# Kernel optimization log

Measured on AMD Instinct MI355X. Metric: run time of the kernel, lower is better.

## Reference

```python
import jax, jax.numpy as jnp
import numpy as np

EPS = 1e-12


def _koleo_single(x):
    # x: [B, D]
    # F.normalize(p=2, dim=-1): x / max(||x||, eps)
    norm = jnp.linalg.norm(x, axis=-1, keepdims=True)
    xn = x / jnp.maximum(norm, EPS)
    # pairwise inner products [B, B], mask diagonal with -1
    dots = xn @ xn.T
    n = xn.shape[0]
    dots = jnp.where(jnp.eye(n, dtype=bool), -1.0, dots)
    I = jnp.argmax(dots, axis=1)  # nearest neighbor index per row
    # torch PairwiseDistance(2, eps): (sum (x - y + eps)^2)^(1/2)
    diff = xn - xn[I] + EPS
    distances = jnp.sqrt(jnp.sum(diff * diff, axis=-1))
    return -jnp.mean(jnp.log(distances + EPS))


def setup_inputs() -> dict:
    key = jax.random.key(0)
    episodes_vectors = jax.random.normal(key, (8192, 4, 1024), dtype=jnp.float32)
    return {"episodes_vectors": episodes_vectors}


def reference(episodes_vectors) -> jnp.ndarray:
    # [B, T, D] -> [T, B, D], one KoLeo loss per view, averaged
    x_tbd = jnp.transpose(episodes_vectors, (1, 0, 2))
    losses = jax.vmap(_koleo_single)(x_tbd)  # [T]
    return jnp.mean(losses)
```

## Files before the change

kernel.cpp:

```cpp
#include <hip/hip_runtime.h>
#include <hip/hip_bf16.h>
#include <math.h>

#define B_N 8192
#define T_N 4
#define D_N 1024
#define BM  128
#define BN  256
#define NT  16
#define NBLK 1056

typedef float f32x4 __attribute__((ext_vector_type(4)));
typedef long longx2 __attribute__((ext_vector_type(2)));

__device__ inline unsigned int f2u_ord(float f) {
    unsigned int b = __float_as_uint(f);
    return (b & 0x80000000u) ? ~b : (b | 0x80000000u);
}
__device__ inline float u2f_ord(unsigned int u) {
    unsigned int b = (u & 0x80000000u) ? (u & 0x7FFFFFFFu) : ~u;
    return __uint_as_float(b);
}

__device__ inline unsigned int f2e4m3(float f) {
    unsigned int u = __float_as_uint(f);
    unsigned int sgn = (u >> 24) & 0x80u;
    int e = (int)((u >> 23) & 0xFFu) - 127;
    unsigned int m = u & 0x7FFFFFu;
    if (e >= -6) {
        unsigned int mant = m >> 20;
        unsigned int rest = m & 0xFFFFFu;
        mant += (rest > 0x80000u) || (rest == 0x80000u && (mant & 1u));
        unsigned int exp8 = (unsigned)(e + 7);
        if (mant == 8u) { mant = 0u; exp8 += 1u; }
        return sgn | (exp8 << 3) | mant;
    } else {
        float a = fabsf(f) * 512.0f;
        int q = (int)rintf(a);
        if (q >= 8) return sgn | 0x08u;
        return sgn | (unsigned)q;
    }
}

__global__ __launch_bounds__(256) void init_rowmax_kernel(unsigned int* __restrict__ rowmax) {
    int i = blockIdx.x * 256 + threadIdx.x;
    if (i < T_N * B_N) rowmax[i] = 0u;
}

__global__ __launch_bounds__(256) void norm_kernel(const float* __restrict__ in,
                                                   unsigned char* __restrict__ xn) {
    const int row  = blockIdx.x * 4 + (threadIdx.x >> 6);
    const int lane = threadIdx.x & 63;
    const int b = row >> 2;
    const int t = row & 3;
    const float* src = in + (size_t)row * D_N;

    float4 v[4];
    float ss = 0.f;
#pragma unroll
    for (int i = 0; i < 4; ++i) {
        v[i] = reinterpret_cast<const float4*>(src)[lane + 64 * i];
        ss += v[i].x * v[i].x + v[i].y * v[i].y + v[i].z * v[i].z + v[i].w * v[i].w;
    }
#pragma unroll
    for (int off = 32; off; off >>= 1) ss += __shfl_xor(ss, off, 64);
    const float rn = 1.0f / fmaxf(sqrtf(ss), 1e-12f);

    unsigned int* dst = reinterpret_cast<unsigned int*>(xn + ((size_t)t * B_N + b) * D_N);
#pragma unroll
    for (int i = 0; i < 4; ++i) {
        unsigned int p = f2e4m3(v[i].x * rn) | (f2e4m3(v[i].y * rn) << 8) |
                         (f2e4m3(v[i].z * rn) << 16) | (f2e4m3(v[i].w * rn) << 24);
        const int w  = lane + 64 * i;
        const int pp = (((w >> 1) & 3) << 1) | ((w >> 3) & 1);
        const int dw = (w & ~15) | (pp << 1) | (w & 1);
        dst[dw] = p;
    }
}

#define GLOAD_LDS16(g, l)                                                              \
    __builtin_amdgcn_global_load_lds(                                                  \
        (const __attribute__((address_space(1))) unsigned int*)(g),                    \
        (__attribute__((address_space(3))) unsigned int*)(l), 16, 0, 0)

__global__ __launch_bounds__(512, 4) void gemm_rowmax_kernel(const unsigned char* __restrict__ xn,
                                                             unsigned int* __restrict__ rowmax) {
    const int t = blockIdx.z;
    const int bid = blockIdx.x;
    int l = (bid & 7) * (NBLK / 8) + (bid >> 3);
    int bx = 0;
    while (l >= 2 * bx + 2) { l -= 2 * bx + 2; ++bx; }
    const int by = l;

    const unsigned char* X = xn + (size_t)t * B_N * D_N;

    __shared__ __align__(16) unsigned char lds[73728];

    const int tid  = threadIdx.x;
    const int lane = tid & 63;
    const int wv   = tid >> 6;
    const int wm   = wv >> 2;
    const int wn   = wv & 3;

    const int srow = lane >> 2;
    const int spos = (lane & 3) ^ ((lane >> 4) & 3);
    const unsigned char* gA  = X + (size_t)(by * BM + wv * 16 + srow) * D_N + spos * 16;
    const unsigned char* gB0 = X + (size_t)(bx * BN + wv * 16 + srow) * D_N + spos * 16;
    const unsigned char* gB1 = gB0 + (size_t)128 * D_N;

    const unsigned rdoff = (unsigned)(lane & 15) * 64u +
                           (unsigned)(((lane >> 4) ^ (lane >> 2)) & 3) * 16u;

    f32x4 acc[4][4];
#pragma unroll
    for (int m = 0; m < 4; ++m)
#pragma unroll
        for (int n = 0; n < 4; ++n) acc[m][n] = (f32x4){0.f, 0.f, 0.f, 0.f};

#define BARRIER asm volatile("s_barrier" ::: "memory")
#define VMCNT(N) asm volatile("s_waitcnt vmcnt(" #N ")" ::: "memory")
#define STAGE(buf, kc)                                                                  \
    GLOAD_LDS16(gA + (kc),  &lds[(buf) + wv * 1024u]);                                  \
    GLOAD_LDS16(gB0 + (kc), &lds[(buf) + 8192u + wv * 1024u]);                          \
    GLOAD_LDS16(gB1 + (kc), &lds[(buf) + 16384u + wv * 1024u]);

    STAGE(0u, 0)
    STAGE(24576u, 64)
    VMCNT(3);

    int cur = 0;
    for (int kt = 0; kt < NT; ++kt) {
        BARRIER;

        if (kt + 2 < NT) {
            int n2 = cur - 1; if (n2 < 0) n2 += 3;
            STAGE((unsigned)n2 * 24576u, (kt + 2) * 64)
        }

        const unsigned bb = (unsigned)cur * 24576u;

        longx2 bV[4];
#pragma unroll
        for (int nf = 0; nf < 4; ++nf) {
            const unsigned rB = bb + 8192u + (unsigned)wn * 4096u + (unsigned)nf * 1024u + rdoff;
            bV[nf] = *reinterpret_cast<const longx2*>(&lds[rB]);
        }
        __builtin_amdgcn_s_setprio(1);
#pragma unroll
        for (int mf = 0; mf < 4; ++mf) {
            const unsigned rA = bb + (unsigned)wm * 4096u + (unsigned)mf * 1024u + rdoff;
            longx2 aV = *reinterpret_cast<const longx2*>(&lds[rA]);
#pragma unroll
            for (int nf = 0; nf < 4; ++nf) {
                acc[mf][nf] = __builtin_amdgcn_mfma_f32_16x16x32_fp8_fp8(
                    aV[0], bV[nf][0], acc[mf][nf], 0, 0, 0);
                acc[mf][nf] = __builtin_amdgcn_mfma_f32_16x16x32_fp8_fp8(
                    aV[1], bV[nf][1], acc[mf][nf], 0, 0, 0);
            }
        }
        __builtin_amdgcn_s_setprio(0);

        if (kt < NT - 2) { VMCNT(3); } else { VMCNT(0); }

        cur = (cur == 2) ? 0 : cur + 1;
    }

    const int rbase = by * BM + wm * 64;
    const int cbase = bx * BN + wn * 64;
    unsigned int* rm = rowmax + t * B_N;

#pragma unroll
    for (int m = 0; m < 4; ++m) {
#pragma unroll
        for (int r = 0; r < 4; ++r) {
            const int row = rbase + m * 16 + (lane >> 4) * 4 + r;
            float mx = -2.0f;
#pragma unroll
            for (int n = 0; n < 4; ++n) {
                const int col = cbase + n * 16 + (lane & 15);
                float v = acc[m][n][r];
                if (col != row) mx = fmaxf(mx, v);
            }
#pragma unroll
            for (int off = 1; off < 16; off <<= 1) mx = fmaxf(mx, __shfl_xor(mx, off, 64));
            if ((lane & 15) == 0) atomicMax(&rm[row], f2u_ord(mx));
        }
    }
#pragma unroll
    for (int n = 0; n < 4; ++n) {
        const int col = cbase + n * 16 + (lane & 15);
        float mx = -2.0f;
#pragma unroll
        for (int m = 0; m < 4; ++m)
#pragma unroll
            for (int r = 0; r < 4; ++r) {
                const int row = rbase + m * 16 + (lane >> 4) * 4 + r;
                float v = acc[m][n][r];
                if (col != row) mx = fmaxf(mx, v);
            }
        mx = fmaxf(mx, __shfl_xor(mx, 16, 64));
        mx = fmaxf(mx, __shfl_xor(mx, 32, 64));
        if ((lane >> 4) == 0) atomicMax(&rm[col], f2u_ord(mx));
    }
#undef BARRIER
#undef VMCNT
#undef STAGE
}

__global__ __launch_bounds__(256) void finish_kernel(const unsigned int* __restrict__ rowmax,
                                                     float* __restrict__ out) {
    __shared__ float sbuf[4];
    float s = 0.f;
    for (int i = threadIdx.x; i < T_N * B_N; i += 256) {
        float m  = u2f_ord(rowmax[i]);
        float d2 = fmaxf(2.0f - 2.0f * m, 0.0f);
        s += logf(sqrtf(d2) + 1e-12f);
    }
#pragma unroll
    for (int off = 32; off; off >>= 1) s += __shfl_xor(s, off, 64);
    const int w = threadIdx.x >> 6;
    if ((threadIdx.x & 63) == 0) sbuf[w] = s;
    __syncthreads();
    if (threadIdx.x == 0) {
        out[0] = -(sbuf[0] + sbuf[1] + sbuf[2] + sbuf[3]) / (float)(T_N * B_N);
    }
}

extern "C" void kernel_launch(void* const* d_in, const int* in_sizes, int n_in,
                              void* d_out, int out_size, void* d_ws, size_t ws_size,
                              hipStream_t stream) {
    const float* in = (const float*)d_in[0];
    unsigned char* xn = (unsigned char*)d_ws;
    unsigned int* rowmax = (unsigned int*)((char*)d_ws + (size_t)T_N * B_N * D_N);
    float* out = (float*)d_out;

    init_rowmax_kernel<<<(T_N * B_N + 255) / 256, 256, 0, stream>>>(rowmax);
    norm_kernel<<<(B_N * T_N) / 4, 256, 0, stream>>>(in, xn);
    dim3 g(NBLK, 1, T_N);
    gemm_rowmax_kernel<<<g, 512, 0, stream>>>(xn, rowmax);
    finish_kernel<<<1, 256, 0, stream>>>(rowmax, out);
}
```

Baseline: 263.2 us.

## Use double-buffered LDS for higher occupancy, fuse rowmax init, parallelize final reduction

```diff
diff --git a/kernel.cpp b/kernel.cpp
--- a/kernel.cpp
+++ b/kernel.cpp
@@ -42,13 +42,11 @@
     }
 }
 
-__global__ __launch_bounds__(256) void init_rowmax_kernel(unsigned int* __restrict__ rowmax) {
-    int i = blockIdx.x * 256 + threadIdx.x;
-    if (i < T_N * B_N) rowmax[i] = 0u;
-}
-
 __global__ __launch_bounds__(256) void norm_kernel(const float* __restrict__ in,
-                                                   unsigned char* __restrict__ xn) {
+                                                   unsigned char* __restrict__ xn,
+                                                   unsigned int* __restrict__ rowmax) {
+    if (blockIdx.x < (T_N * B_N) / 256) rowmax[blockIdx.x * 256 + threadIdx.x] = 0u;
+
     const int row  = blockIdx.x * 4 + (threadIdx.x >> 6);
     const int lane = threadIdx.x & 63;
     const int b = row >> 2;
@@ -83,7 +81,7 @@
         (const __attribute__((address_space(1))) unsigned int*)(g),                    \
         (__attribute__((address_space(3))) unsigned int*)(l), 16, 0, 0)
 
-__global__ __launch_bounds__(512, 4) void gemm_rowmax_kernel(const unsigned char* __restrict__ xn,
+__global__ __launch_bounds__(512, 6) void gemm_rowmax_kernel(const unsigned char* __restrict__ xn,
                                                              unsigned int* __restrict__ rowmax) {
     const int t = blockIdx.z;
     const int bid = blockIdx.x;
@@ -94,7 +92,7 @@
 
     const unsigned char* X = xn + (size_t)t * B_N * D_N;
 
-    __shared__ __align__(16) unsigned char lds[73728];
+    __shared__ __align__(16) unsigned char lds[49152];
 
     const int tid  = threadIdx.x;
     const int lane = tid & 63;
@@ -125,19 +123,15 @@
     GLOAD_LDS16(gB1 + (kc), &lds[(buf) + 16384u + wv * 1024u]);
 
     STAGE(0u, 0)
-    STAGE(24576u, 64)
-    VMCNT(3);
-
-    int cur = 0;
+    VMCNT(0);
+
     for (int kt = 0; kt < NT; ++kt) {
+        const unsigned bb = (kt & 1) ? 24576u : 0u;
+        const unsigned bw = (kt & 1) ? 0u : 24576u;
+
         BARRIER;
 
-        if (kt + 2 < NT) {
-            int n2 = cur - 1; if (n2 < 0) n2 += 3;
-            STAGE((unsigned)n2 * 24576u, (kt + 2) * 64)
-        }
-
-        const unsigned bb = (unsigned)cur * 24576u;
+        if (kt + 1 < NT) { STAGE(bw, (kt + 1) * 64) }
 
         longx2 bV[4];
 #pragma unroll
@@ -160,9 +154,7 @@
         }
         __builtin_amdgcn_s_setprio(0);
 
-        if (kt < NT - 2) { VMCNT(3); } else { VMCNT(0); }
-
-        cur = (cur == 2) ? 0 : cur + 1;
+        VMCNT(0);
     }
 
     const int rbase = by * BM + wm * 64;
@@ -207,11 +199,11 @@
 #undef STAGE
 }
 
-__global__ __launch_bounds__(256) void finish_kernel(const unsigned int* __restrict__ rowmax,
-                                                     float* __restrict__ out) {
+__global__ __launch_bounds__(256) void finish_partial_kernel(const unsigned int* __restrict__ rowmax,
+                                                             float* __restrict__ partials) {
     __shared__ float sbuf[4];
     float s = 0.f;
-    for (int i = threadIdx.x; i < T_N * B_N; i += 256) {
+    for (int i = blockIdx.x * 256 + threadIdx.x; i < T_N * B_N; i += 64 * 256) {
         float m  = u2f_ord(rowmax[i]);
         float d2 = fmaxf(2.0f - 2.0f * m, 0.0f);
         s += logf(sqrtf(d2) + 1e-12f);
@@ -221,9 +213,15 @@
     const int w = threadIdx.x >> 6;
     if ((threadIdx.x & 63) == 0) sbuf[w] = s;
     __syncthreads();
-    if (threadIdx.x == 0) {
-        out[0] = -(sbuf[0] + sbuf[1] + sbuf[2] + sbuf[3]) / (float)(T_N * B_N);
-    }
+    if (threadIdx.x == 0) partials[blockIdx.x] = sbuf[0] + sbuf[1] + sbuf[2] + sbuf[3];
+}
+
+__global__ __launch_bounds__(64) void finish_final_kernel(const float* __restrict__ partials,
+                                                          float* __restrict__ out) {
+    float s = partials[threadIdx.x];
+#pragma unroll
+    for (int off = 32; off; off >>= 1) s += __shfl_xor(s, off, 64);
+    if (threadIdx.x == 0) out[0] = -s / (float)(T_N * B_N);
 }
 
 extern "C" void kernel_launch(void* const* d_in, const int* in_sizes, int n_in,
@@ -232,11 +230,12 @@
     const float* in = (const float*)d_in[0];
     unsigned char* xn = (unsigned char*)d_ws;
     unsigned int* rowmax = (unsigned int*)((char*)d_ws + (size_t)T_N * B_N * D_N);
+    float* partials = (float*)((char*)d_ws + (size_t)T_N * B_N * D_N + (size_t)T_N * B_N * 4);
     float* out = (float*)d_out;
 
-    init_rowmax_kernel<<<(T_N * B_N + 255) / 256, 256, 0, stream>>>(rowmax);
-    norm_kernel<<<(B_N * T_N) / 4, 256, 0, stream>>>(in, xn);
+    norm_kernel<<<(B_N * T_N) / 4, 256, 0, stream>>>(in, xn, rowmax);
     dim3 g(NBLK, 1, T_N);
     gemm_rowmax_kernel<<<g, 512, 0, stream>>>(xn, rowmax);
-    finish_kernel<<<1, 256, 0, stream>>>(rowmax, out);
-}
+    finish_partial_kernel<<<64, 256, 0, stream>>>(rowmax, partials);
+    finish_final_kernel<<<1, 64, 0, stream>>>(partials, out);
+}
```

Measured after the change: 977.2 us. 3.71x slower.
